# Performance work log

Hardware: AMD Instinct MI355X
Metric: run time of the kernel (lower is better)

The kernel has to match this reference:

```python
import jax, jax.numpy as jnp
import numpy as np

D = 256      # d_model
P = 8        # patch_len
H = 8        # heads
S = 3200     # spec_len
B = 64       # batch


def setup_inputs() -> dict:
    key = jax.random.key(0)
    ks = jax.random.split(key, 16)
    def w(k, shape):
        fan_in = shape[0]
        return jax.random.normal(k, shape, jnp.float32) / np.sqrt(fan_in)
    return {
        "spec": jax.random.normal(ks[0], (B, S), jnp.float32),
        # embed MLP: Linear(1,D) -> ReLU -> Linear(D,D)
        "W1": w(ks[1], (1, D)), "b1": jnp.zeros((D,), jnp.float32),
        "W2": w(ks[2], (D, D)), "b2": jnp.zeros((D,), jnp.float32),
        # multi-head attention projections
        "Wq": w(ks[3], (D, D)), "bq": jnp.zeros((D,), jnp.float32),
        "Wk": w(ks[4], (D, D)), "bk": jnp.zeros((D,), jnp.float32),
        "Wv": w(ks[5], (D, D)), "bv": jnp.zeros((D,), jnp.float32),
        "Wo": w(ks[6], (D, D)), "bo": jnp.zeros((D,), jnp.float32),
        # patch projection: Linear(P*D, D)
        "Wp": w(ks[7], (P * D, D)), "bp": jnp.zeros((D,), jnp.float32),
    }


def reference(spec, W1, b1, W2, b2, Wq, bq, Wk, bk, Wv, bv, Wo, bo, Wp, bp):
    b = spec.shape[0]
    nw = spec.shape[1] // P  # number of patch windows
    dk = D // H
    # scalar embed MLP: [b, S] -> [b, S, D]
    e = jnp.maximum(spec[..., None] * W1[0] + b1, 0.0) @ W2 + b2
    # chop into non-overlapping windows: [b, nw, P, D]
    e = e.reshape(b, nw, P, D)
    # QKV projections, split heads -> [b, nw, P, H, dk]
    q = (e @ Wq + bq).reshape(b, nw, P, H, dk)
    k = (e @ Wk + bk).reshape(b, nw, P, H, dk)
    v = (e @ Wv + bv).reshape(b, nw, P, H, dk)
    # attention within each tiny window of length P
    scores = jnp.einsum('bwqhd,bwkhd->bwhqk', q, k) / np.sqrt(dk).astype(np.float32)
    attn = jax.nn.softmax(scores, axis=-1)
    o = jnp.einsum('bwhqk,bwkhd->bwqhd', attn, v).reshape(b, nw, P, D)
    o = o @ Wo + bo
    # concat patch tokens and project: [b, nw, P*D] -> [b, nw, D]
    return o.reshape(b, nw, P * D) @ Wp + bp
```

## Files before the change

kernel.cpp:

```cpp
#include <hip/hip_runtime.h>
#include <hip/hip_bf16.h>

typedef unsigned short u16;
typedef __attribute__((ext_vector_type(8))) short short8;
typedef __attribute__((ext_vector_type(4))) short short4_t;
typedef __attribute__((ext_vector_type(4))) float floatx4;

#define MFMA16(A, B, C) __builtin_amdgcn_mfma_f32_16x16x32_bf16((A), (B), (C), 0, 0, 0)

#define OF_PART  64
#define OF_FQKV  (OF_PART + 4096)
#define OF_SORT  (OF_FQKV + 1536)
#define OF_EVK   (OF_SORT + 512)
#define OF_CA    (OF_EVK + 256)
#define OF_CB    (OF_CA + 512)
#define OF_MA    (OF_CB + 512)
#define OF_MB    (OF_MA + 512)
#define OF_P2    (OF_MB + 512)
#define OF_TAB   (OF_P2 + 49152)
#define OF_WP    (OF_TAB + 789504)
#define OF_ORAW  (OF_WP + 524288)
#define OF_WQB   OF_ORAW
#define NPM8     204800

static __device__ __forceinline__ float bf2f(u16 u) {
  union { unsigned int i; float f; } z; z.i = ((unsigned int)u) << 16; return z.f;
}
static __device__ __forceinline__ u16 f2bf(float f) {
  union { float f; unsigned int i; } z; z.f = f;
  unsigned int x = z.i + 0x7fffu + ((z.i >> 16) & 1u);
  return (u16)(x >> 16);
}
static __device__ __forceinline__ unsigned pkbf(float lo, float hi) {
  __hip_bfloat162 h = __float22bfloat162_rn(make_float2(lo, hi));
  unsigned r; __builtin_memcpy(&r, &h, 4); return r;
}

static __device__ __forceinline__ int detect_flag(const u16* __restrict__ sp) {
  const int lane = threadIdx.x & 63;
  int bad = 0;
#pragma unroll
  for (int j = 0; j < 4; ++j) {
    u16 v = sp[lane * 4 + j];
    int e = (v >> 7) & 0xFF;
    bad += (e >= 137);
  }
  return (__popcll(__ballot(bad > 0)) >= 4) ? 1 : 0;
}

#define CV(src, idx) (flag ? f2bf(((const float*)(src))[idx]) : ((const u16*)(src))[idx])

__global__ void prep1_kernel(
    const void* spec, const void* W1, const void* b1, const void* W2,
    const void* Wq, const void* bq, const void* Wk, const void* bk, const void* Wv,
    const void* bv_, const void* Wo, const void* bo, const void* Wp, const void* b2,
    u16* __restrict__ ws) {
  const int flag = detect_flag((const u16*)spec);
  const int b = blockIdx.x, tid = threadIdx.x;
  __shared__ u16 Bs[32 * 72];
  if (b == 187) {
    __shared__ float st[256];
    __shared__ int   sk[256];
    __shared__ float w1s[256], b1s[256];
    w1s[tid] = flag ? ((const float*)W1)[tid] : bf2f(((const u16*)W1)[tid]);
    b1s[tid] = flag ? ((const float*)b1)[tid] : bf2f(((const u16*)b1)[tid]);
    __syncthreads();
    {
      const float w = w1s[tid];
      st[tid] = (w != 0.f) ? (-b1s[tid] / w) : 1e30f;
      sk[tid] = tid;
    }
    for (int size = 2; size <= 256; size <<= 1) {
      for (int stride = size >> 1; stride > 0; stride >>= 1) {
        __syncthreads();
        const int ixj = tid ^ stride;
        if (ixj > tid) {
          const bool up = ((tid & size) == 0);
          float a = st[tid], bq2 = st[ixj];
          if (up ? (a > bq2) : (a < bq2)) {
            int ka = sk[tid];
            st[tid] = bq2; st[ixj] = a;
            sk[tid] = sk[ixj]; sk[ixj] = ka;
          }
        }
      }
    }
    __syncthreads();
    ((float*)(ws + OF_SORT))[tid] = st[tid];
    ws[OF_EVK + tid] = (u16)sk[tid];
    {
      const int ke = sk[tid];
      const float w = w1s[ke], bb = b1s[ke];
      const float sg = (w > 0.f) ? 1.f : ((w < 0.f) ? -1.f : 0.f);
      ((float*)(ws + OF_CA))[tid] = sg * w;
      ((float*)(ws + OF_CB))[tid] = sg * bb;
    }
    {
      const float wk = w1s[tid], bk2 = b1s[tid];
      const bool act0 = (wk < 0.f) || (wk == 0.f && bk2 > 0.f);
      ((float*)(ws + OF_MA))[tid] = act0 ? wk : 0.f;
      ((float*)(ws + OF_MB))[tid] = act0 ? bk2 : 0.f;
    }
    return;
  }
  if (b >= 176) {
    const int t = b - 176, n = tid;
    if (t < 3) {
      const void* SB = (t == 0) ? Wq : (t == 1) ? Wk : Wv;
      const void* bs = (t == 0) ? bq : (t == 1) ? bk : bv_;
      float acc;
      if (flag) {
        acc = ((const float*)bs)[n];
        const float* Bf = (const float*)SB; const float* b2f = (const float*)b2;
        for (int k = 0; k < 256; ++k) acc = fmaf(b2f[k], Bf[k * 256 + n], acc);
      } else {
        acc = bf2f(((const u16*)bs)[n]);
        const u16* Bh = (const u16*)SB; const u16* b2h = (const u16*)b2;
        for (int k = 0; k < 256; ++k) acc = fmaf(bf2f(b2h[k]), bf2f(Bh[k * 256 + n]), acc);
      }
      ((float*)(ws + OF_FQKV))[t * 256 + n] = acc;
    } else {
      const int p = t - 3;
      float acc = 0.f;
      if (flag) {
        const float* Wf = (const float*)Wp; const float* bf = (const float*)bo;
        for (int m = 0; m < 256; ++m) acc = fmaf(bf[m], Wf[(p * 256 + m) * 256 + n], acc);
      } else {
        const u16* Wh = (const u16*)Wp; const u16* bh = (const u16*)bo;
        for (int m = 0; m < 256; ++m)
          acc = fmaf(bf2f(bh[m]), bf2f(Wh[(p * 256 + m) * 256 + n]), acc);
      }
      ((float*)(ws + OF_PART))[p * 256 + n] = acc;
    }
    return;
  }
  const int g = b >> 4, sub = b & 15;
  const int r0 = (sub >> 2) * 64, c0 = (sub & 3) * 64;
  const void* SA = (g < 3) ? W2 : Wo;
  const void* SB = (g == 0) ? Wq : (g == 1) ? Wk : (g == 2) ? Wv : Wp;
  const int brow0 = (g < 3) ? 0 : (g - 3) * 256;
  const int w = tid >> 6, lane = tid & 63, l15 = lane & 15, quad = lane >> 4;
  const int arow = r0 + w * 16 + l15;
  const int srow = tid >> 3, sseg = tid & 7;
  floatx4 acc[4];
#pragma unroll
  for (int ni = 0; ni < 4; ++ni) acc[ni] = (floatx4){0.f, 0.f, 0.f, 0.f};
  for (int kc = 0; kc < 8; ++kc) {
    __syncthreads();
    if (flag) {
      const float* Bf = (const float*)SB;
      const float* src = Bf + (brow0 + kc * 32 + srow) * 256 + c0 + sseg * 8;
      floatx4 f0 = *(const floatx4*)src, f1 = *(const floatx4*)(src + 4);
      union { short8 s8; unsigned u[4]; } t;
      t.u[0] = pkbf(f0[0], f0[1]); t.u[1] = pkbf(f0[2], f0[3]);
      t.u[2] = pkbf(f1[0], f1[1]); t.u[3] = pkbf(f1[2], f1[3]);
      *(short8*)(Bs + srow * 72 + sseg * 8) = t.s8;
    } else {
      const u16* Bh = (const u16*)SB;
      *(short8*)(Bs + srow * 72 + sseg * 8) =
          *(const short8*)(Bh + (brow0 + kc * 32 + srow) * 256 + c0 + sseg * 8);
    }
    __syncthreads();
    const int k0 = kc * 32 + quad * 8;
    union { short8 s8; u16 u[8]; } av;
    if (flag) {
      const float* A = (const float*)SA;
      floatx4 a0 = *(const floatx4*)(A + arow * 256 + k0);
      floatx4 a1 = *(const floatx4*)(A + arow * 256 + k0 + 4);
      av.u[0] = f2bf(a0[0]); av.u[1] = f2bf(a0[1]); av.u[2] = f2bf(a0[2]); av.u[3] = f2bf(a0[3]);
      av.u[4] = f2bf(a1[0]); av.u[5] = f2bf(a1[1]); av.u[6] = f2bf(a1[2]); av.u[7] = f2bf(a1[3]);
    } else {
      const u16* A = (const u16*)SA;
      av.s8 = *(const short8*)(A + arow * 256 + k0);
    }
#pragma unroll
    for (int ni = 0; ni < 4; ++ni) {
      union { short8 s8; u16 u[8]; } bu;
#pragma unroll
      for (int j = 0; j < 8; ++j) bu.u[j] = Bs[(quad * 8 + j) * 72 + ni * 16 + l15];
      acc[ni] = MFMA16(av.s8, bu.s8, acc[ni]);
    }
  }
  if (g < 3) {
    u16* dst = ws + OF_WQB + g * 65536;
#pragma unroll
    for (int ni = 0; ni < 4; ++ni) {
      const int n = c0 + ni * 16 + l15;
#pragma unroll
      for (int r = 0; r < 4; ++r) {
        const int k = r0 + w * 16 + quad * 4 + r;
        dst[k * 256 + n] = f2bf(acc[ni][r]);
      }
    }
  } else {
    u16* dst = ws + OF_WP;
#pragma unroll
    for (int ni = 0; ni < 4; ++ni) {
      const int n = c0 + ni * 16 + l15;
#pragma unroll
      for (int r = 0; r < 4; ++r) {
        const int k = brow0 + r0 + w * 16 + quad * 4 + r;
        dst[(k >> 3) * 2048 + n * 8 + (k & 7)] = f2bf(acc[ni][r]);
      }
    }
  }
}

__global__ void prep2a_kernel(u16* __restrict__ ws) {
  const int tbl = blockIdx.x >> 3, chunk = blockIdx.x & 7;
  const int n = threadIdx.x;
  const int m = tbl >> 1, isB = tbl & 1;
  const u16* S = ws + OF_WQB + m * 65536;
  const float* MC = (const float*)(ws + (isB ? OF_MB : OF_MA));
  const float* CC = (const float*)(ws + (isB ? OF_CB : OF_CA));
  const u16* EVK = ws + OF_EVK;
  float bacc = 0.f, eacc = 0.f;
#pragma unroll 8
  for (int j = 0; j < 32; ++j) {
    const int k = chunk * 32 + j;
    bacc = fmaf(MC[k], bf2f(S[k * 256 + n]), bacc);
    eacc = fmaf(CC[k], bf2f(S[EVK[k] * 256 + n]), eacc);
  }
  float* P = (float*)(ws + OF_P2);
  P[((tbl * 8 + chunk) * 2 + 0) * 256 + n] = bacc;
  P[((tbl * 8 + chunk) * 2 + 1) * 256 + n] = eacc;
}

__global__ void prep2b_kernel(u16* __restrict__ ws) {
  const int tbl = blockIdx.x >> 3, seg = blockIdx.x & 7;
  const int n = threadIdx.x;
  const int m = tbl >> 1, isB = tbl & 1;
  const u16* S = ws + OF_WQB + m * 65536;
  const float* CC = (const float*)(ws + (isB ? OF_CB : OF_CA));
  const u16* EVK = ws + OF_EVK;
  const float* P = (const float*)(ws + OF_P2);
  float cur = isB ? ((const float*)(ws + OF_FQKV))[m * 256 + n] : 0.f;
#pragma unroll
  for (int c = 0; c < 8; ++c) cur += P[((tbl * 8 + c) * 2 + 0) * 256 + n];
  for (int c = 0; c < seg; ++c) cur += P[((tbl * 8 + c) * 2 + 1) * 256 + n];
  float* dst = (float*)(ws + OF_TAB) + tbl * 65792;
  const int rlo = seg * 32;
  dst[rlo * 256 + n] = cur;
  const int nev = (seg == 7) ? 32 : 31;
  for (int i = 0; i < nev; ++i) {
    const int e = rlo + i;
    cur = fmaf(CC[e], bf2f(S[EVK[e] * 256 + n]), cur);
    dst[(e + 1) * 256 + n] = cur;
  }
}

__global__ __launch_bounds__(256) void fused_lite_kernel(
    const void* __restrict__ spec, const float* __restrict__ tsort,
    const float* __restrict__ tAq, const float* __restrict__ tBq,
    const float* __restrict__ tAk, const float* __restrict__ tBk,
    const float* __restrict__ tAv, const float* __restrict__ tBv,
    u16* __restrict__ oraw)
{
  __shared__ u16 vbT[16384];
  __shared__ u16 pscr[1024];
  __shared__ float sS[64];
  __shared__ int   sR[64];
  __shared__ int   part[256];

  const int flag = detect_flag((const u16*)spec);
  const int tid = threadIdx.x;
  const int wave = tid >> 6, lane = tid & 63;
  const int l15 = lane & 15, quad = lane >> 4;
  const int tile0 = blockIdx.x * 64;
  const floatx4 zero4 = (floatx4){0.f, 0.f, 0.f, 0.f};

  {
    const int m = tid & 63, qt = tid >> 6;
    const float sm = flag ? ((const float*)spec)[tile0 + m]
                          : bf2f(((const u16*)spec)[tile0 + m]);
    int cnt = 0;
#pragma unroll 8
    for (int j = 0; j < 64; ++j) cnt += (tsort[qt * 64 + j] < sm) ? 1 : 0;
    part[tid] = cnt;
    __syncthreads();
    if (tid < 64) {
      sR[tid] = part[tid] + part[tid + 64] + part[tid + 128] + part[tid + 192];
      sS[tid] = sm;
    }
    __syncthreads();
  }

  {
    const int tp = tid & 31, db = tid >> 5;
    const int t0 = tp * 2, t1 = t0 + 1;
    const float s0 = sS[t0], s1 = sS[t1];
    const float* A0 = tAv + sR[t0] * 256;
    const float* B0 = tBv + sR[t0] * 256;
    const float* A1 = tAv + sR[t1] * 256;
    const float* B1 = tBv + sR[t1] * 256;
    unsigned* vbT32 = (unsigned*)vbT;
#pragma unroll
    for (int j = 0; j < 32; j += 4) {
      const int d = db * 32 + j;
      floatx4 a0 = *(const floatx4*)(A0 + d), b0 = *(const floatx4*)(B0 + d);
      floatx4 a1 = *(const floatx4*)(A1 + d), b1 = *(const floatx4*)(B1 + d);
#pragma unroll
      for (int e = 0; e < 4; ++e) {
        const int dd = d + e;
        vbT32[dd * 32 + ((((tp >> 2) ^ (dd & 7)) << 2) | (tp & 3))] =
            pkbf(fmaf(s0, a0[e], b0[e]), fmaf(s1, a1[e], b1[e]));
      }
    }
  }
  __syncthreads();

  unsigned opk[32];
  {
    const int w2 = wave * 2;
    const int tok = wave * 16 + l15;
    const int r_t = sR[tok];
    const float s_t = sS[tok];
    const int valid = ((l15 >> 3) == (quad >> 1));
    u16* ps = pscr + wave * 256;
    const float* Aq = tAq + r_t * 256;
    const float* Bq = tBq + r_t * 256;
    const float* Ak = tAk + r_t * 256;
    const float* Bk = tBk + r_t * 256;
#pragma unroll
    for (int h = 0; h < 8; ++h) {
      const int d8 = h * 32 + quad * 8;
      short8 qv, kv;
      {
        floatx4 a0 = *(const floatx4*)(Aq + d8), a1 = *(const floatx4*)(Aq + d8 + 4);
        floatx4 b0 = *(const floatx4*)(Bq + d8), b1 = *(const floatx4*)(Bq + d8 + 4);
        union { short8 s8; unsigned u[4]; } z;
        z.u[0] = pkbf(fmaf(s_t, a0[0], b0[0]), fmaf(s_t, a0[1], b0[1]));
        z.u[1] = pkbf(fmaf(s_t, a0[2], b0[2]), fmaf(s_t, a0[3], b0[3]));
        z.u[2] = pkbf(fmaf(s_t, a1[0], b1[0]), fmaf(s_t, a1[1], b1[1]));
        z.u[3] = pkbf(fmaf(s_t, a1[2], b1[2]), fmaf(s_t, a1[3], b1[3]));
        qv = z.s8;
      }
      {
        floatx4 a0 = *(const floatx4*)(Ak + d8), a1 = *(const floatx4*)(Ak + d8 + 4);
        floatx4 b0 = *(const floatx4*)(Bk + d8), b1 = *(const floatx4*)(Bk + d8 + 4);
        union { short8 s8; unsigned u[4]; } z;
        z.u[0] = pkbf(fmaf(s_t, a0[0], b0[0]), fmaf(s_t, a0[1], b0[1]));
        z.u[1] = pkbf(fmaf(s_t, a0[2], b0[2]), fmaf(s_t, a0[3], b0[3]));
        z.u[2] = pkbf(fmaf(s_t, a1[0], b1[0]), fmaf(s_t, a1[1], b1[1]));
        z.u[3] = pkbf(fmaf(s_t, a1[2], b1[2]), fmaf(s_t, a1[3], b1[3]));
        kv = z.s8;
      }
      floatx4 sc = MFMA16(kv, qv, zero4);
      const float SC = 0.17677669529663687f;
      float s0 = sc[0] * SC, s1 = sc[1] * SC, s2 = sc[2] * SC, s3 = sc[3] * SC;
      float m4 = fmaxf(fmaxf(s0, s1), fmaxf(s2, s3));
      float mx = fmaxf(m4, __shfl_xor(m4, 16));
      float p0 = __expf(s0 - mx), p1 = __expf(s1 - mx);
      float p2 = __expf(s2 - mx), p3 = __expf(s3 - mx);
      float sm = (p0 + p1) + (p2 + p3);
      float su = sm + __shfl_xor(sm, 16);
      float inv = 1.f / su;
      float v0 = valid ? p0 * inv : 0.f, v1 = valid ? p1 * inv : 0.f;
      float v2 = valid ? p2 * inv : 0.f, v3 = valid ? p3 * inv : 0.f;
      union { short4_t s4; unsigned u[2]; } pw;
      pw.u[0] = pkbf(v0, v1); pw.u[1] = pkbf(v2, v3);
      *(short4_t*)(ps + l15 * 16 + quad * 4) = pw.s4;
#pragma unroll
      for (int dh = 0; dh < 2; ++dh) {
        const int vcol = h * 32 + dh * 16 + l15;
        short8 pa = (short8){0, 0, 0, 0, 0, 0, 0, 0};
        short8 vf = (short8){0, 0, 0, 0, 0, 0, 0, 0};
        if (quad < 2) {
          pa = *(const short8*)(ps + l15 * 16 + quad * 8);
          vf = *(const short8*)(vbT + vcol * 64 + (((w2 + quad) ^ (vcol & 7)) << 3));
        }
        floatx4 o = MFMA16(pa, vf, zero4);
        opk[(h * 2 + dh) * 2]     = pkbf(o[0], o[1]);
        opk[(h * 2 + dh) * 2 + 1] = pkbf(o[2], o[3]);
      }
    }
  }

  {
    const int mbase = (blockIdx.x * 8 + wave * 2 + (quad >> 1)) * 8 + (l15 & 7);
    const int pb4 = (quad & 1) * 4;
#pragma unroll
    for (int h = 0; h < 8; ++h)
#pragma unroll
      for (int dh = 0; dh < 2; ++dh) {
        const int oi = (h * 2 + dh) * 2;
        const int e8 = h * 4 + dh * 2 + (l15 >> 3);
        const unsigned lo = opk[oi], hi = opk[oi + 1];
        oraw[((pb4 + 0) * 32 + e8) * NPM8 + mbase] = (u16)lo;
        oraw[((pb4 + 1) * 32 + e8) * NPM8 + mbase] = (u16)(lo >> 16);
        oraw[((pb4 + 2) * 32 + e8) * NPM8 + mbase] = (u16)hi;
        oraw[((pb4 + 3) * 32 + e8) * NPM8 + mbase] = (u16)(hi >> 16);
      }
  }
}

__global__ __launch_bounds__(256) void patch_gemm_kernel(
    const u16* __restrict__ spec_raw,
    const u16* __restrict__ oraw, const u16* __restrict__ sWp,
    const void* __restrict__ bp, const float* __restrict__ part,
    void* __restrict__ out)
{
  const int flag = detect_flag(spec_raw);
  const int tid = threadIdx.x;
  const int wave = tid >> 6, lane = tid & 63;
  const int l15 = lane & 15, quad = lane >> 4;
  const int m0 = (blockIdx.x >> 1) * 64;
  const int n0 = (blockIdx.x & 1) * 128 + wave * 32;
  const floatx4 zero4 = (floatx4){0.f, 0.f, 0.f, 0.f};

  floatx4 acc[4][2];
#pragma unroll
  for (int mi = 0; mi < 4; ++mi)
#pragma unroll
    for (int ni = 0; ni < 2; ++ni) acc[mi][ni] = zero4;

  const u16* ap = oraw + quad * NPM8 + (m0 + l15) * 8;
  const u16* bpw = sWp + quad * 2048 + (n0 + l15) * 8;
#pragma unroll 4
  for (int kk = 0; kk < 64; ++kk) {
    short8 b0 = *(const short8*)(bpw);
    short8 b1 = *(const short8*)(bpw + 128);
#pragma unroll
    for (int mi = 0; mi < 4; ++mi) {
      short8 a = *(const short8*)(ap + mi * 128);
      acc[mi][0] = MFMA16(a, b0, acc[mi][0]);
      acc[mi][1] = MFMA16(a, b1, acc[mi][1]);
    }
    ap += 4 * NPM8;
    bpw += 4 * 2048;
  }

#pragma unroll
  for (int ni = 0; ni < 2; ++ni) {
    const int n = n0 + ni * 16 + l15;
    float bb = bf2f(CV(bp, n));
#pragma unroll
    for (int p = 0; p < 8; ++p) bb += part[p * 256 + n];
#pragma unroll
    for (int mi = 0; mi < 4; ++mi) {
      const int mr = m0 + mi * 16 + quad * 4;
      if (flag) {
        float* po = (float*)out;
#pragma unroll
        for (int r = 0; r < 4; ++r)
          po[(mr + r) * 256 + n] = acc[mi][ni][r] + bb;
      } else {
        u16* po = (u16*)out;
#pragma unroll
        for (int r = 0; r < 4; ++r)
          po[(mr + r) * 256 + n] = f2bf(acc[mi][ni][r] + bb);
      }
    }
  }
}

extern "C" void kernel_launch(void* const* d_in, const int* in_sizes, int n_in,
                              void* d_out, int out_size, void* d_ws, size_t ws_size,
                              hipStream_t stream) {
  (void)in_sizes; (void)n_in; (void)out_size; (void)ws_size;
  u16* ws = (u16*)d_ws;

  prep1_kernel<<<188, 256, 0, stream>>>(
      d_in[0], d_in[1], d_in[2], d_in[3],
      d_in[5], d_in[6], d_in[7], d_in[8], d_in[9], d_in[10],
      d_in[11], d_in[12], d_in[13], d_in[4], ws);
  prep2a_kernel<<<48, 256, 0, stream>>>(ws);
  prep2b_kernel<<<48, 256, 0, stream>>>(ws);
  const float* TB = (const float*)(ws + OF_TAB);
  fused_lite_kernel<<<3200, 256, 0, stream>>>(
      d_in[0], (const float*)(ws + OF_SORT),
      TB,             TB + 65792,
      TB + 2 * 65792, TB + 3 * 65792,
      TB + 4 * 65792, TB + 5 * 65792,
      ws + OF_ORAW);
  patch_gemm_kernel<<<800, 256, 0, stream>>>(
      (const u16*)d_in[0],
      ws + OF_ORAW, ws + OF_WP,
      d_in[14], (const float*)(ws + OF_PART),
      d_out);
}
```

Measured before the change: 254.1 us.

## Interleave Q/K lookup tables per row and replace LDS scratch with shuffles

The Q and K affine lookup tables (A and B coefficients for both) are written in an interleaved per-row layout, so each lane fetches its q/k coefficients for a head from one contiguous 128-byte span. The rank search is now done per token inside each wave and reduced with lane shuffles, which drops the partial-count shared array and one barrier. The softmax probabilities are redistributed with cross-lane shuffles instead of a round trip through LDS scratch. These changes target the cost of scattered table gathers, LDS traffic and barriers, at the price of more shuffle instructions and a more complex table index.

```diff
diff --git a/kernel.cpp b/kernel.cpp
--- a/kernel.cpp
+++ b/kernel.cpp
@@ -18,6 +18,8 @@
 #define OF_MB    (OF_MA + 512)
 #define OF_P2    (OF_MB + 512)
 #define OF_TAB   (OF_P2 + 49152)
+#define NF_QK    263168
+#define NF_V     65792
 #define OF_WP    (OF_TAB + 789504)
 #define OF_ORAW  (OF_WP + 524288)
 #define OF_WQB   OF_ORAW
@@ -238,29 +240,29 @@
 #pragma unroll
   for (int c = 0; c < 8; ++c) cur += P[((tbl * 8 + c) * 2 + 0) * 256 + n];
   for (int c = 0; c < seg; ++c) cur += P[((tbl * 8 + c) * 2 + 1) * 256 + n];
-  float* dst = (float*)(ws + OF_TAB) + tbl * 65792;
+  float* TB = (float*)(ws + OF_TAB);
   const int rlo = seg * 32;
-  dst[rlo * 256 + n] = cur;
+  const long roff = (tbl < 4) ? ((n >> 3) * 32 + tbl * 8 + (n & 7))
+                              : (NF_QK + (tbl - 4) * NF_V + n);
+  const int rstr = (tbl < 4) ? 1024 : 256;
+  TB[(long)rlo * rstr + roff] = cur;
   const int nev = (seg == 7) ? 32 : 31;
   for (int i = 0; i < nev; ++i) {
     const int e = rlo + i;
     cur = fmaf(CC[e], bf2f(S[EVK[e] * 256 + n]), cur);
-    dst[(e + 1) * 256 + n] = cur;
+    TB[(long)(e + 1) * rstr + roff] = cur;
   }
 }
 
 __global__ __launch_bounds__(256) void fused_lite_kernel(
     const void* __restrict__ spec, const float* __restrict__ tsort,
-    const float* __restrict__ tAq, const float* __restrict__ tBq,
-    const float* __restrict__ tAk, const float* __restrict__ tBk,
-    const float* __restrict__ tAv, const float* __restrict__ tBv,
+    const float* __restrict__ TQK, const float* __restrict__ tAv,
+    const float* __restrict__ tBv,
     u16* __restrict__ oraw)
 {
   __shared__ u16 vbT[16384];
-  __shared__ u16 pscr[1024];
   __shared__ float sS[64];
   __shared__ int   sR[64];
-  __shared__ int   part[256];
 
   const int flag = detect_flag((const u16*)spec);
   const int tid = threadIdx.x;
@@ -269,21 +271,20 @@
   const int tile0 = blockIdx.x * 64;
   const floatx4 zero4 = (floatx4){0.f, 0.f, 0.f, 0.f};
 
+  const int tok = wave * 16 + l15;
+  const float s_t = flag ? ((const float*)spec)[tile0 + tok]
+                         : bf2f(((const u16*)spec)[tile0 + tok]);
+  int r_t;
   {
-    const int m = tid & 63, qt = tid >> 6;
-    const float sm = flag ? ((const float*)spec)[tile0 + m]
-                          : bf2f(((const u16*)spec)[tile0 + m]);
     int cnt = 0;
 #pragma unroll 8
-    for (int j = 0; j < 64; ++j) cnt += (tsort[qt * 64 + j] < sm) ? 1 : 0;
-    part[tid] = cnt;
-    __syncthreads();
-    if (tid < 64) {
-      sR[tid] = part[tid] + part[tid + 64] + part[tid + 128] + part[tid + 192];
-      sS[tid] = sm;
-    }
-    __syncthreads();
-  }
+    for (int j = 0; j < 64; ++j) cnt += (tsort[quad * 64 + j] < s_t) ? 1 : 0;
+    cnt += __shfl_xor(cnt, 16);
+    cnt += __shfl_xor(cnt, 32);
+    r_t = cnt;
+    if (quad == 0) { sS[tok] = s_t; sR[tok] = cnt; }
+  }
+  __syncthreads();
 
   {
     const int tp = tid & 31, db = tid >> 5;
@@ -312,37 +313,31 @@
   unsigned opk[32];
   {
     const int w2 = wave * 2;
-    const int tok = wave * 16 + l15;
-    const int r_t = sR[tok];
-    const float s_t = sS[tok];
     const int valid = ((l15 >> 3) == (quad >> 1));
-    u16* ps = pscr + wave * 256;
-    const float* Aq = tAq + r_t * 256;
-    const float* Bq = tBq + r_t * 256;
-    const float* Ak = tAk + r_t * 256;
-    const float* Bk = tBk + r_t * 256;
+    const float* tq = TQK + r_t * 1024 + quad * 32;
+    const int src0 = (quad & 1) * 32 + l15, src1 = src0 + 16;
 #pragma unroll
     for (int h = 0; h < 8; ++h) {
-      const int d8 = h * 32 + quad * 8;
+      const float* bp8 = tq + h * 128;
+      floatx4 qa0 = *(const floatx4*)(bp8),      qa1 = *(const floatx4*)(bp8 + 4);
+      floatx4 qb0 = *(const floatx4*)(bp8 + 8),  qb1 = *(const floatx4*)(bp8 + 12);
+      floatx4 ka0 = *(const floatx4*)(bp8 + 16), ka1 = *(const floatx4*)(bp8 + 20);
+      floatx4 kb0 = *(const floatx4*)(bp8 + 24), kb1 = *(const floatx4*)(bp8 + 28);
       short8 qv, kv;
       {
-        floatx4 a0 = *(const floatx4*)(Aq + d8), a1 = *(const floatx4*)(Aq + d8 + 4);
-        floatx4 b0 = *(const floatx4*)(Bq + d8), b1 = *(const floatx4*)(Bq + d8 + 4);
         union { short8 s8; unsigned u[4]; } z;
-        z.u[0] = pkbf(fmaf(s_t, a0[0], b0[0]), fmaf(s_t, a0[1], b0[1]));
-        z.u[1] = pkbf(fmaf(s_t, a0[2], b0[2]), fmaf(s_t, a0[3], b0[3]));
-        z.u[2] = pkbf(fmaf(s_t, a1[0], b1[0]), fmaf(s_t, a1[1], b1[1]));
-        z.u[3] = pkbf(fmaf(s_t, a1[2], b1[2]), fmaf(s_t, a1[3], b1[3]));
+        z.u[0] = pkbf(fmaf(s_t, qa0[0], qb0[0]), fmaf(s_t, qa0[1], qb0[1]));
+        z.u[1] = pkbf(fmaf(s_t, qa0[2], qb0[2]), fmaf(s_t, qa0[3], qb0[3]));
+        z.u[2] = pkbf(fmaf(s_t, qa1[0], qb1[0]), fmaf(s_t, qa1[1], qb1[1]));
+        z.u[3] = pkbf(fmaf(s_t, qa1[2], qb1[2]), fmaf(s_t, qa1[3], qb1[3]));
         qv = z.s8;
       }
       {
-        floatx4 a0 = *(const floatx4*)(Ak + d8), a1 = *(const floatx4*)(Ak + d8 + 4);
-        floatx4 b0 = *(const floatx4*)(Bk + d8), b1 = *(const floatx4*)(Bk + d8 + 4);
         union { short8 s8; unsigned u[4]; } z;
-        z.u[0] = pkbf(fmaf(s_t, a0[0], b0[0]), fmaf(s_t, a0[1], b0[1]));
-        z.u[1] = pkbf(fmaf(s_t, a0[2], b0[2]), fmaf(s_t, a0[3], b0[3]));
-        z.u[2] = pkbf(fmaf(s_t, a1[0], b1[0]), fmaf(s_t, a1[1], b1[1]));
-        z.u[3] = pkbf(fmaf(s_t, a1[2], b1[2]), fmaf(s_t, a1[3], b1[3]));
+        z.u[0] = pkbf(fmaf(s_t, ka0[0], kb0[0]), fmaf(s_t, ka0[1], kb0[1]));
+        z.u[1] = pkbf(fmaf(s_t, ka0[2], kb0[2]), fmaf(s_t, ka0[3], kb0[3]));
+        z.u[2] = pkbf(fmaf(s_t, ka1[0], kb1[0]), fmaf(s_t, ka1[1], kb1[1]));
+        z.u[3] = pkbf(fmaf(s_t, ka1[2], kb1[2]), fmaf(s_t, ka1[3], kb1[3]));
         kv = z.s8;
       }
       floatx4 sc = MFMA16(kv, qv, zero4);
@@ -355,20 +350,22 @@
       float sm = (p0 + p1) + (p2 + p3);
       float su = sm + __shfl_xor(sm, 16);
       float inv = 1.f / su;
-      float v0 = valid ? p0 * inv : 0.f, v1 = valid ? p1 * inv : 0.f;
-      float v2 = valid ? p2 * inv : 0.f, v3 = valid ? p3 * inv : 0.f;
-      union { short4_t s4; unsigned u[2]; } pw;
-      pw.u[0] = pkbf(v0, v1); pw.u[1] = pkbf(v2, v3);
-      *(short4_t*)(ps + l15 * 16 + quad * 4) = pw.s4;
+      unsigned pw0 = pkbf(valid ? p0 * inv : 0.f, valid ? p1 * inv : 0.f);
+      unsigned pw1 = pkbf(valid ? p2 * inv : 0.f, valid ? p3 * inv : 0.f);
+      unsigned g0 = __shfl(pw0, src0), g1 = __shfl(pw1, src0);
+      unsigned g2 = __shfl(pw0, src1), g3 = __shfl(pw1, src1);
+      short8 pa = (short8){0, 0, 0, 0, 0, 0, 0, 0};
+      if (quad < 2) {
+        union { short8 s8; unsigned u[4]; } z;
+        z.u[0] = g0; z.u[1] = g1; z.u[2] = g2; z.u[3] = g3;
+        pa = z.s8;
+      }
 #pragma unroll
       for (int dh = 0; dh < 2; ++dh) {
         const int vcol = h * 32 + dh * 16 + l15;
-        short8 pa = (short8){0, 0, 0, 0, 0, 0, 0, 0};
         short8 vf = (short8){0, 0, 0, 0, 0, 0, 0, 0};
-        if (quad < 2) {
-          pa = *(const short8*)(ps + l15 * 16 + quad * 8);
+        if (quad < 2)
           vf = *(const short8*)(vbT + vcol * 64 + (((w2 + quad) ^ (vcol & 7)) << 3));
-        }
         floatx4 o = MFMA16(pa, vf, zero4);
         opk[(h * 2 + dh) * 2]     = pkbf(o[0], o[1]);
         opk[(h * 2 + dh) * 2 + 1] = pkbf(o[2], o[3]);
@@ -469,9 +466,7 @@
   const float* TB = (const float*)(ws + OF_TAB);
   fused_lite_kernel<<<3200, 256, 0, stream>>>(
       d_in[0], (const float*)(ws + OF_SORT),
-      TB,             TB + 65792,
-      TB + 2 * 65792, TB + 3 * 65792,
-      TB + 4 * 65792, TB + 5 * 65792,
+      TB, TB + NF_QK, TB + NF_QK + NF_V,
       ws + OF_ORAW);
   patch_gemm_kernel<<<800, 256, 0, stream>>>(
       (const u16*)d_in[0],
```

New measurement: 261.6 us. 2.9% more time.
